# Performance work log

Measured on AMD Instinct MI355X. Metric: run time of the kernel, lower is better.

The kernel has to match this reference:

```python
import jax, jax.numpy as jnp
import numpy as np
import math

MODEL_DIM = 2048
NUM_EXPERTS = 64
N_TOKENS = 16384
CAPACITY_FACTOR = 1.0
MIN_CAPACITY = 8
THRESHOLD = 0.5


def _threshold_gating(logits):
    # Faithful jax translation of main_thresholdGating (training path, threshold>0).
    # Note: the torch code truncates sorted columns to the data-dependent
    # explore_top_k_num; we keep the full E columns instead. This is exactly
    # equivalent: dropped columns are all-unchosen (importance 0), and using
    # arange(E,0,-1) instead of arange(K,0,-1) shifts every chosen importance
    # by the same constant (E-K), which preserves the per-expert top-k order.
    N, E = logits.shape
    capacity = max(int(math.ceil(N / E * CAPACITY_FACTOR)), MIN_CAPACITY)  # static

    gates = jax.nn.softmax(logits, axis=1)                    # [N,E]
    indices1 = jnp.argmax(gates, axis=1)                      # top-1 expert per token
    mask1 = jax.nn.one_hot(indices1, E, dtype=gates.dtype)    # [N,E]

    # sorted gates + cumsum threshold selection
    gates_sorted, gates_idx = jax.lax.top_k(gates, E)         # [N,E] descending
    cum = jnp.cumsum(gates_sorted, axis=-1)
    chosen = (cum - gates_sorted) < THRESHOLD                 # [N,E] bool
    chosen = chosen.at[:, 0].set(True)                        # always keep top-1

    # scatter importance = rank-priority + gate prob into expert columns
    rank_imp = jnp.arange(E, 0, -1, dtype=gates.dtype)[None, :] + gates_sorted
    imp = jnp.where(chosen, rank_imp, jnp.zeros_like(rank_imp))
    row = jnp.arange(N)[:, None]
    # gates_idx rows are permutations of experts -> no scatter collisions
    tam = jnp.zeros((N, E), gates.dtype).at[row, gates_idx].set(imp)  # [N,E]

    # capacity truncation: per expert column keep the `capacity` tokens with
    # highest importance
    top_idx = jax.lax.top_k(tam.T, capacity)[1]               # [E, capacity]
    keep = jnp.zeros((N, E), gates.dtype).at[top_idx, jnp.arange(E)[:, None]].set(1.0)
    final_mask = ((tam * keep) > 0).astype(gates.dtype)       # [N,E]

    combine_weights = gates * final_mask

    # load-balancing aux loss (GShard style)
    me = jnp.mean(gates, axis=0)
    ce = jnp.mean(mask1, axis=0)
    l_aux = jnp.sum(me * ce) * E
    return l_aux, combine_weights


def setup_inputs() -> dict:
    key = jax.random.key(0)
    kx, kw = jax.random.split(key)
    x = jax.random.normal(kx, (N_TOKENS, MODEL_DIM), dtype=jnp.float32)
    # gate weight of wg = Linear(model_dim, num_experts, bias=False)
    W = jax.random.normal(kw, (NUM_EXPERTS, MODEL_DIM), dtype=jnp.float32) / math.sqrt(MODEL_DIM)
    return {"x": x, "W": W}


def reference(x, W):
    logits = x @ W.T                                          # [N,E]
    l_aux, combine_weights = _threshold_gating(logits)
    return l_aux, combine_weights
```

## Files before the change

kernel.cpp:

```cpp
#include <hip/hip_runtime.h>
#include <cstdint>
#include <cstddef>

#define N_TOK  16384
#define NEXP   64
#define KDIM   2048
#define CAP    256
#define NE_TOT ((size_t)N_TOK * NEXP)

typedef __attribute__((ext_vector_type(8))) short short8;
typedef __attribute__((ext_vector_type(4))) float f32x4;
typedef __attribute__((ext_vector_type(4))) unsigned int uint4x;

__device__ __forceinline__ unsigned short bf16_rtn(float f) {
  unsigned u = __float_as_uint(f);
  u += 0x7FFFu + ((u >> 16) & 1u);
  return (unsigned short)(u >> 16);
}
__device__ __forceinline__ float bf16_f(unsigned short h) {
  return __uint_as_float((unsigned)h << 16);
}
__device__ __forceinline__ f32x4 MF(short8 a, short8 b, f32x4 c) {
  return __builtin_amdgcn_mfma_f32_16x16x32_bf16(a, b, c, 0, 0, 0);
}
__device__ __forceinline__ unsigned cvt_pk(float a, float b) {
  unsigned r;
  asm("v_cvt_pk_bf16_f32 %0, %1, %2" : "=v"(r) : "v"(a), "v"(b));
  return r;
}
__device__ __forceinline__ float lo16f(unsigned u) {
  return __uint_as_float(u << 16);
}
__device__ __forceinline__ float hi16f(unsigned u) {
  return __uint_as_float(u & 0xFFFF0000u);
}

__global__ __launch_bounds__(256) void wdigits(const float* __restrict__ W,
    unsigned short* __restrict__ Wh, unsigned short* __restrict__ Wl,
    unsigned short* __restrict__ Wq) {
  const int e = (int)blockIdx.x * 256 + (int)threadIdx.x;
  const int col = e >> 11;
  const int k   = e & 2047;
  const float w = W[(size_t)col * KDIM + k];
  const unsigned short h = bf16_rtn(w);
  const float r1 = w - bf16_f(h);
  const unsigned short lo = bf16_rtn(r1);
  const float r2 = r1 - bf16_f(lo);
  const unsigned short q = bf16_rtn(r2);
  const size_t idx = (size_t)(k >> 3) * 512 + (size_t)col * 8 + (k & 7);
  Wh[idx] = h; Wl[idx] = lo; Wq[idx] = q;
}

__device__ __forceinline__ void cvt8pk(float4 a, float4 b,
                                       short8& h, short8& lo, short8& q) {
  const float f0 = a.x, f1 = a.y, f2 = a.z, f3 = a.w;
  const float f4 = b.x, f5 = b.y, f6 = b.z, f7 = b.w;
  const unsigned h0 = cvt_pk(f0, f1), h1 = cvt_pk(f2, f3);
  const unsigned h2 = cvt_pk(f4, f5), h3 = cvt_pk(f6, f7);
  const float r0 = f0 - lo16f(h0), r1 = f1 - hi16f(h0);
  const float r2 = f2 - lo16f(h1), r3 = f3 - hi16f(h1);
  const float r4 = f4 - lo16f(h2), r5 = f5 - hi16f(h2);
  const float r6 = f6 - lo16f(h3), r7 = f7 - hi16f(h3);
  const unsigned l0 = cvt_pk(r0, r1), l1 = cvt_pk(r2, r3);
  const unsigned l2 = cvt_pk(r4, r5), l3 = cvt_pk(r6, r7);
  const float s0 = r0 - lo16f(l0), s1 = r1 - hi16f(l0);
  const float s2 = r2 - lo16f(l1), s3 = r3 - hi16f(l1);
  const float s4 = r4 - lo16f(l2), s5 = r5 - hi16f(l2);
  const float s6 = r6 - lo16f(l3), s7 = r7 - hi16f(l3);
  const unsigned q0 = cvt_pk(s0, s1), q1 = cvt_pk(s2, s3);
  const unsigned q2 = cvt_pk(s4, s5), q3 = cvt_pk(s6, s7);
  h  = __builtin_bit_cast(short8, (uint4x){h0, h1, h2, h3});
  lo = __builtin_bit_cast(short8, (uint4x){l0, l1, l2, l3});
  q  = __builtin_bit_cast(short8, (uint4x){q0, q1, q2, q3});
}

template <int KS>
__global__ __launch_bounds__(256) void gemm_mfma(const float* __restrict__ x,
    const unsigned short* __restrict__ Wh, const unsigned short* __restrict__ Wl,
    const unsigned short* __restrict__ Wq, float* __restrict__ part) {
  constexpr int NSTEP = (KDIM / KS) / 32;
  const int tid = (int)threadIdx.x;
  const int l   = tid & 63;
  const int wv  = tid >> 6;
  const int ks  = (int)blockIdx.x % KS;
  const int mt  = (int)blockIdx.x / KS;
  const int row0 = mt * 256 + wv * 64;
  const int kBeg = ks * (KDIM / KS);
  const int lr = l & 15;
  const int lk = l >> 4;

  f32x4 acc[4][4];
#pragma unroll
  for (int rt = 0; rt < 4; ++rt)
#pragma unroll
    for (int cb = 0; cb < 4; ++cb) acc[rt][cb] = (f32x4){0.f, 0.f, 0.f, 0.f};

  const float* pa0 = x + (size_t)(row0 + lr) * KDIM + kBeg + lk * 8;
  const size_t bbase = ((size_t)((kBeg >> 3) + lk)) * 64 + lr;
  const short8* BH = (const short8*)Wh + bbase;
  const short8* BL = (const short8*)Wl + bbase;
  const short8* BQ = (const short8*)Wq + bbase;

  float4 Ac[4][2];
#pragma unroll
  for (int rt = 0; rt < 4; ++rt) {
    const float* p = pa0 + (size_t)rt * 16 * KDIM;
    Ac[rt][0] = *(const float4*)p;
    Ac[rt][1] = *(const float4*)(p + 4);
  }

  for (int s = 0; s < NSTEP; ++s) {
    const int so = s * 256;
    short8 bh[4], bl[4], bq[4];
#pragma unroll
    for (int cb = 0; cb < 4; ++cb) {
      bh[cb] = BH[so + cb * 16];
      bl[cb] = BL[so + cb * 16];
      bq[cb] = BQ[so + cb * 16];
    }
    float4 An[4][2];
    if (s + 1 < NSTEP) {
      const int ko = (s + 1) * 32;
#pragma unroll
      for (int rt = 0; rt < 4; ++rt) {
        const float* p = pa0 + (size_t)rt * 16 * KDIM + ko;
        An[rt][0] = *(const float4*)p;
        An[rt][1] = *(const float4*)(p + 4);
      }
    }
    short8 ah[4], al[4], aq[4];
#pragma unroll
    for (int rt = 0; rt < 4; ++rt)
      cvt8pk(Ac[rt][0], Ac[rt][1], ah[rt], al[rt], aq[rt]);

#pragma unroll
    for (int cb = 0; cb < 4; ++cb) {
#pragma unroll
      for (int rt = 0; rt < 4; ++rt) {
        acc[rt][cb] = MF(ah[rt], bh[cb], acc[rt][cb]);
        acc[rt][cb] = MF(ah[rt], bl[cb], acc[rt][cb]);
        acc[rt][cb] = MF(al[rt], bh[cb], acc[rt][cb]);
        acc[rt][cb] = MF(al[rt], bl[cb], acc[rt][cb]);
        acc[rt][cb] = MF(aq[rt], bh[cb], acc[rt][cb]);
        acc[rt][cb] = MF(ah[rt], bq[cb], acc[rt][cb]);
      }
    }

    if (s + 1 < NSTEP) {
#pragma unroll
      for (int rt = 0; rt < 4; ++rt) { Ac[rt][0] = An[rt][0]; Ac[rt][1] = An[rt][1]; }
    }
  }

  float* pout = part + (size_t)ks * NE_TOT;
#pragma unroll
  for (int rt = 0; rt < 4; ++rt) {
    const int rb = row0 + rt * 16 + lk * 4;
#pragma unroll
    for (int r = 0; r < 4; ++r) {
#pragma unroll
      for (int cb = 0; cb < 4; ++cb)
        pout[(size_t)(rb + r) * 64 + cb * 16 + lr] = acc[rt][cb][r];
    }
  }
}

template <int KS>
__global__ __launch_bounds__(1024) void gate_rows(const float* __restrict__ part,
                                                  float* __restrict__ gatesT,
                                                  float* __restrict__ tamT) {
  __shared__ float gt[64][65];
  __shared__ float tt[64][65];
  const int tid  = (int)threadIdx.x;
  const int lane = tid & 63;
  const int wid  = tid >> 6;
  const int row0 = (int)blockIdx.x * 64;

#pragma unroll
  for (int r = 0; r < 4; ++r) {
    const int rloc = wid * 4 + r;
    const size_t base = (size_t)(row0 + rloc) * NEXP;

    float logit = 0.f;
#pragma unroll
    for (int s = 0; s < KS; ++s)
      logit += part[(size_t)s * NE_TOT + base + lane];

    float m = logit;
#pragma unroll
    for (int off = 32; off > 0; off >>= 1) m = fmaxf(m, __shfl_xor(m, off));
    float p = expf(logit - m);
    float sum = p;
#pragma unroll
    for (int off = 32; off > 0; off >>= 1) sum += __shfl_xor(sum, off);
    const float gate = p / sum;

    float g = gate;
    int idx = lane;
#pragma unroll
    for (int k = 2; k <= 64; k <<= 1) {
#pragma unroll
      for (int j = k >> 1; j > 0; j >>= 1) {
        float og = __shfl_xor(g, j);
        int   oi = __shfl_xor(idx, j);
        bool iLower     = (lane & j) == 0;
        bool wantFirst  = ((lane & k) == 0) ? iLower : !iLower;
        bool otherFirst = (og > g) || (og == g && oi < idx);
        if (otherFirst == wantFirst) { g = og; idx = oi; }
      }
    }

    float cum = g;
#pragma unroll
    for (int off = 1; off < 64; off <<= 1) {
      float t = __shfl_up(cum, off);
      if (lane >= off) cum += t;
    }
    const bool chosen = (lane == 0) || ((cum - g) < 0.5f);
    const float imp = chosen ? ((float)(NEXP - lane) + g) : 0.f;

    gt[rloc][lane] = gate;
    tt[rloc][idx]  = imp;
  }
  __syncthreads();

#pragma unroll
  for (int p = 0; p < 4; ++p) {
    const int e = p * 16 + wid;
    gatesT[(size_t)e * N_TOK + row0 + lane] = gt[lane][e];
    tamT  [(size_t)e * N_TOK + row0 + lane] = tt[lane][e];
  }
}

__global__ __launch_bounds__(1024) void expert_select(
    const float* __restrict__ gatesT, const float* __restrict__ tamT,
    float* __restrict__ me_sum, int* __restrict__ ce_cnt,
    float* __restrict__ combT) {
  __shared__ int   hist16[16][256];
  __shared__ int   hist[256];
  __shared__ float wsum[16];
  __shared__ int   wice[16];
  __shared__ int   wnnz[16];
  __shared__ int   wcnt[16];
  __shared__ unsigned sh_prefix;
  __shared__ int      sh_k;
  __shared__ int      sh_nnz;

  const int e    = (int)blockIdx.x;
  const int tid  = (int)threadIdx.x;
  const int lane = tid & 63;
  const int wid  = tid >> 6;
  const float* tcol = tamT   + (size_t)e * N_TOK;
  const float* gcol = gatesT + (size_t)e * N_TOK;

  float gsum = 0.f;
  int ccnt = 0, nnzl = 0;
#pragma unroll
  for (int k = 0; k < 4; ++k) {
    int i4 = tid + k * 1024;
    float4 tv = reinterpret_cast<const float4*>(tcol)[i4];
    float4 gv = reinterpret_cast<const float4*>(gcol)[i4];
    gsum += gv.x + gv.y + gv.z + gv.w;
    ccnt += (tv.x > 64.f) + (tv.y > 64.f) + (tv.z > 64.f) + (tv.w > 64.f);
    nnzl += (tv.x != 0.f) + (tv.y != 0.f) + (tv.z != 0.f) + (tv.w != 0.f);
  }
#pragma unroll
  for (int off = 32; off > 0; off >>= 1) {
    gsum += __shfl_xor(gsum, off);
    ccnt += __shfl_xor(ccnt, off);
    nnzl += __shfl_xor(nnzl, off);
  }
  if (lane == 0) { wsum[wid] = gsum; wice[wid] = ccnt; wnnz[wid] = nnzl; }
  __syncthreads();
  if (tid == 0) {
    float t = 0.f; int c = 0, nz = 0;
    for (int w = 0; w < 16; ++w) { t += wsum[w]; c += wice[w]; nz += wnnz[w]; }
    me_sum[e] = t; ce_cnt[e] = c; sh_nnz = nz;
  }
  __syncthreads();
  const int nnz = sh_nnz;

  unsigned vstar = 0u;
  int meq = 0;
  if (nnz > CAP) {
    unsigned prefix = 0;
    int krem = CAP;
    for (int round = 0; round < 4; ++round) {
      const int shift = 24 - 8 * round;
      const unsigned maskAbove =
          (round == 0) ? 0u : (0xFFFFFFFFu << (shift + 8));
      for (int z = tid; z < 16 * 256; z += 1024) ((int*)hist16)[z] = 0;
      __syncthreads();
#pragma unroll
      for (int k = 0; k < 16; ++k) {
        unsigned u = __float_as_uint(tcol[tid + k * 1024]);
        if (u != 0u && (u & maskAbove) == prefix)
          atomicAdd(&hist16[wid][(u >> shift) & 255], 1);
      }
      __syncthreads();
      if (tid < 256) {
        int s = 0;
#pragma unroll
        for (int w = 0; w < 16; ++w) s += hist16[w][tid];
        hist[tid] = s;
      }
      __syncthreads();
      if (wid == 0) {
        int h0 = hist[lane * 4 + 0], h1 = hist[lane * 4 + 1];
        int h2 = hist[lane * 4 + 2], h3 = hist[lane * 4 + 3];
        int lsum = h0 + h1 + h2 + h3;
        int suf = lsum;
#pragma unroll
        for (int off = 1; off < 64; off <<= 1) {
          int t = __shfl_down(suf, off);
          if (lane + off < 64) suf += t;
        }
        int above = suf - lsum;
        int S3 = above + h3, S2 = S3 + h2, S1 = S2 + h1, S0 = S1 + h0;
        if (S0 >= krem && S1    < krem) { sh_prefix = prefix | ((unsigned)(lane*4+0) << shift); sh_k = krem - S1;    }
        if (S1 >= krem && S2    < krem) { sh_prefix = prefix | ((unsigned)(lane*4+1) << shift); sh_k = krem - S2;    }
        if (S2 >= krem && S3    < krem) { sh_prefix = prefix | ((unsigned)(lane*4+2) << shift); sh_k = krem - S3;    }
        if (S3 >= krem && above < krem) { sh_prefix = prefix | ((unsigned)(lane*4+3) << shift); sh_k = krem - above; }
      }
      __syncthreads();
      prefix = sh_prefix;
      krem   = sh_k;
      __syncthreads();
    }
    vstar = prefix;
    meq   = krem;
  }

  float4 tq[4];
#pragma unroll
  for (int q = 0; q < 4; ++q)
    tq[q] = reinterpret_cast<const float4*>(tcol)[tid * 4 + q];
  int cnt = 0;
#pragma unroll
  for (int q = 0; q < 4; ++q) {
    cnt += (__float_as_uint(tq[q].x) == vstar);
    cnt += (__float_as_uint(tq[q].y) == vstar);
    cnt += (__float_as_uint(tq[q].z) == vstar);
    cnt += (__float_as_uint(tq[q].w) == vstar);
  }
  int inc = cnt;
#pragma unroll
  for (int off = 1; off < 64; off <<= 1) {
    int t = __shfl_up(inc, off);
    if (lane >= off) inc += t;
  }
  if (lane == 63) wcnt[wid] = inc;
  __syncthreads();
  if (tid == 0) {
    int run = 0;
    for (int w = 0; w < 16; ++w) { int t = wcnt[w]; wcnt[w] = run; run += t; }
  }
  __syncthreads();
  int exc = (inc - cnt) + wcnt[wid];

  float* ccol = combT + (size_t)e * N_TOK;
#pragma unroll
  for (int q = 0; q < 4; ++q) {
    float4 gq = reinterpret_cast<const float4*>(gcol)[tid * 4 + q];
    float ov[4];
    const float tv[4] = {tq[q].x, tq[q].y, tq[q].z, tq[q].w};
    const float gv[4] = {gq.x, gq.y, gq.z, gq.w};
#pragma unroll
    for (int j = 0; j < 4; ++j) {
      unsigned u = __float_as_uint(tv[j]);
      bool keep;
      if (u == vstar) { keep = (exc < meq); ++exc; }
      else            { keep = (u > vstar); }
      ov[j] = (keep && u != 0u) ? gv[j] : 0.f;
    }
    reinterpret_cast<float4*>(ccol)[tid * 4 + q] =
        make_float4(ov[0], ov[1], ov[2], ov[3]);
  }
}

__global__ __launch_bounds__(1024) void transpose_out(
    const float* __restrict__ combT, float* __restrict__ out1,
    const float* __restrict__ me_sum, const int* __restrict__ ce_cnt,
    float* __restrict__ out0) {
  __shared__ float tile[64][65];
  const int tid  = (int)threadIdx.x;
  const int lane = tid & 63;
  const int wid  = tid >> 6;
  const int tok0 = (int)blockIdx.x * 64;
#pragma unroll
  for (int p = 0; p < 4; ++p) {
    const int e = p * 16 + wid;
    tile[lane][e] = combT[(size_t)e * N_TOK + tok0 + lane];
  }
  __syncthreads();
#pragma unroll
  for (int q = 0; q < 4; ++q) {
    const int tok = q * 16 + wid;
    out1[(size_t)(tok0 + tok) * NEXP + lane] = tile[tok][lane];
  }
  if (blockIdx.x == 0 && wid == 0) {
    float v = (me_sum[lane] / (float)N_TOK) *
              ((float)ce_cnt[lane] / (float)N_TOK);
#pragma unroll
    for (int off = 32; off > 0; off >>= 1) v += __shfl_xor(v, off);
    if (lane == 0) out0[0] = v * (float)NEXP;
  }
}

extern "C" void kernel_launch(void* const* d_in, const int* in_sizes, int n_in,
                              void* d_out, int out_size, void* d_ws, size_t ws_size,
                              hipStream_t stream) {
  const float* x = (const float*)d_in[0];
  const float* W = (const float*)d_in[1];
  float* out = (float*)d_out;
  float* ws  = (float*)d_ws;

  const bool ks8 = ws_size >= (size_t)(8 + 2) * NE_TOT * 4 + 1024;

  const int KS = ks8 ? 8 : 4;
  float* part   = ws;
  float* combT  = ws;
  float* gatesT = ws + (size_t)KS * NE_TOT;
  float* tamT   = gatesT + NE_TOT;
  float* me     = tamT + NE_TOT;
  int*   ce     = (int*)(me + 64);

  unsigned short* Wh = (unsigned short*)gatesT;
  unsigned short* Wl = Wh + (size_t)NEXP * KDIM;
  unsigned short* Wq = Wl + (size_t)NEXP * KDIM;

  wdigits<<<(NEXP * KDIM) / 256, 256, 0, stream>>>(W, Wh, Wl, Wq);
  if (ks8) gemm_mfma<8><<<64 * 8, 256, 0, stream>>>(x, Wh, Wl, Wq, part);
  else     gemm_mfma<4><<<64 * 4, 256, 0, stream>>>(x, Wh, Wl, Wq, part);
  if (ks8) gate_rows<8><<<N_TOK / 64, 1024, 0, stream>>>(part, gatesT, tamT);
  else     gate_rows<4><<<N_TOK / 64, 1024, 0, stream>>>(part, gatesT, tamT);
  expert_select<<<NEXP, 1024, 0, stream>>>(gatesT, tamT, me, ce, combT);
  transpose_out<<<N_TOK / 64, 1024, 0, stream>>>(combT, out + 1, me, ce, out);
}
```

Measured before the change: 73.95 us.

## Stage x tile through double-buffered LDS with coalesced global loads

```diff
diff --git a/kernel.cpp b/kernel.cpp
--- a/kernel.cpp
+++ b/kernel.cpp
@@ -79,13 +79,15 @@
     const unsigned short* __restrict__ Wh, const unsigned short* __restrict__ Wl,
     const unsigned short* __restrict__ Wq, float* __restrict__ part) {
   constexpr int NSTEP = (KDIM / KS) / 32;
+  __shared__ float As[2][9216];
   const int tid = (int)threadIdx.x;
   const int l   = tid & 63;
   const int wv  = tid >> 6;
   const int ks  = (int)blockIdx.x % KS;
   const int mt  = (int)blockIdx.x / KS;
-  const int row0 = mt * 256 + wv * 64;
-  const int kBeg = ks * (KDIM / KS);
+  const int row0b = mt * 256;
+  const int row0  = row0b + wv * 64;
+  const int kBeg  = ks * (KDIM / KS);
   const int lr = l & 15;
   const int lk = l >> 4;
 
@@ -95,21 +97,32 @@
 #pragma unroll
     for (int cb = 0; cb < 4; ++cb) acc[rt][cb] = (f32x4){0.f, 0.f, 0.f, 0.f};
 
-  const float* pa0 = x + (size_t)(row0 + lr) * KDIM + kBeg + lk * 8;
+  const int sgr = tid >> 3;
+  const int sch = tid & 7;
+  const float* sp = x + (size_t)(row0b + sgr) * KDIM + kBeg + sch * 4;
+
   const size_t bbase = ((size_t)((kBeg >> 3) + lk)) * 64 + lr;
   const short8* BH = (const short8*)Wh + bbase;
   const short8* BL = (const short8*)Wl + bbase;
   const short8* BQ = (const short8*)Wq + bbase;
 
-  float4 Ac[4][2];
-#pragma unroll
-  for (int rt = 0; rt < 4; ++rt) {
-    const float* p = pa0 + (size_t)rt * 16 * KDIM;
-    Ac[rt][0] = *(const float4*)p;
-    Ac[rt][1] = *(const float4*)(p + 4);
-  }
+  float4 st[8];
+#pragma unroll
+  for (int p = 0; p < 8; ++p)
+    st[p] = *(const float4*)(sp + (size_t)p * 32 * KDIM);
+#pragma unroll
+  for (int p = 0; p < 8; ++p)
+    *(float4*)&As[0][(sgr + p * 32) * 36 + sch * 4] = st[p];
+  __syncthreads();
 
   for (int s = 0; s < NSTEP; ++s) {
+    const int buf = s & 1;
+    if (s + 1 < NSTEP) {
+      const int ko = (s + 1) * 32;
+#pragma unroll
+      for (int p = 0; p < 8; ++p)
+        st[p] = *(const float4*)(sp + (size_t)p * 32 * KDIM + ko);
+    }
     const int so = s * 256;
     short8 bh[4], bl[4], bq[4];
 #pragma unroll
@@ -118,20 +131,14 @@
       bl[cb] = BL[so + cb * 16];
       bq[cb] = BQ[so + cb * 16];
     }
-    float4 An[4][2];
-    if (s + 1 < NSTEP) {
-      const int ko = (s + 1) * 32;
-#pragma unroll
-      for (int rt = 0; rt < 4; ++rt) {
-        const float* p = pa0 + (size_t)rt * 16 * KDIM + ko;
-        An[rt][0] = *(const float4*)p;
-        An[rt][1] = *(const float4*)(p + 4);
-      }
-    }
     short8 ah[4], al[4], aq[4];
 #pragma unroll
-    for (int rt = 0; rt < 4; ++rt)
-      cvt8pk(Ac[rt][0], Ac[rt][1], ah[rt], al[rt], aq[rt]);
+    for (int rt = 0; rt < 4; ++rt) {
+      const float* pb = &As[buf][(wv * 64 + rt * 16 + lr) * 36 + lk * 8];
+      float4 A0 = *(const float4*)pb;
+      float4 A1 = *(const float4*)(pb + 4);
+      cvt8pk(A0, A1, ah[rt], al[rt], aq[rt]);
+    }
 
 #pragma unroll
     for (int cb = 0; cb < 4; ++cb) {
@@ -148,8 +155,10 @@
 
     if (s + 1 < NSTEP) {
 #pragma unroll
-      for (int rt = 0; rt < 4; ++rt) { Ac[rt][0] = An[rt][0]; Ac[rt][1] = An[rt][1]; }
-    }
+      for (int p = 0; p < 8; ++p)
+        *(float4*)&As[buf ^ 1][(sgr + p * 32) * 36 + sch * 4] = st[p];
+    }
+    __syncthreads();
   }
 
   float* pout = part + (size_t)ks * NE_TOT;
```

Measured after the change: 87.41 us. 1.18x slower.

## Stage x tiles through LDS with async global_load_lds double buffering

Applied to the files above, without the earlier changes.

```diff
diff --git a/kernel.cpp b/kernel.cpp
--- a/kernel.cpp
+++ b/kernel.cpp
@@ -79,6 +79,7 @@
     const unsigned short* __restrict__ Wh, const unsigned short* __restrict__ Wl,
     const unsigned short* __restrict__ Wq, float* __restrict__ part) {
   constexpr int NSTEP = (KDIM / KS) / 32;
+  __shared__ float xs[2][4][2048];
   const int tid = (int)threadIdx.x;
   const int l   = tid & 63;
   const int wv  = tid >> 6;
@@ -95,21 +96,36 @@
 #pragma unroll
     for (int cb = 0; cb < 4; ++cb) acc[rt][cb] = (f32x4){0.f, 0.f, 0.f, 0.f};
 
-  const float* pa0 = x + (size_t)(row0 + lr) * KDIM + kBeg + lk * 8;
+  const int srow = l >> 3;
+  const int sch  = (l & 7) ^ srow;
+  const float* sp = x + (size_t)(row0 + srow) * KDIM + kBeg + sch * 4;
+
+  const int m7  = lr & 7;
+  const int c0o = ((lk * 2)     ^ m7) * 4;
+  const int c1o = ((lk * 2 + 1) ^ m7) * 4;
+
   const size_t bbase = ((size_t)((kBeg >> 3) + lk)) * 64 + lr;
   const short8* BH = (const short8*)Wh + bbase;
   const short8* BL = (const short8*)Wl + bbase;
   const short8* BQ = (const short8*)Wq + bbase;
 
-  float4 Ac[4][2];
-#pragma unroll
-  for (int rt = 0; rt < 4; ++rt) {
-    const float* p = pa0 + (size_t)rt * 16 * KDIM;
-    Ac[rt][0] = *(const float4*)p;
-    Ac[rt][1] = *(const float4*)(p + 4);
-  }
+#define STAGE(buf, koff)                                                     \
+  {                                                                          \
+    _Pragma("unroll")                                                        \
+    for (int i_ = 0; i_ < 8; ++i_) {                                         \
+      __builtin_amdgcn_global_load_lds(                                      \
+          sp + (size_t)(i_ * 8) * KDIM + (koff),                             \
+          &xs[(buf)][wv][i_ * 256], 16, 0, 0);                               \
+    }                                                                        \
+  }
+
+  STAGE(0, 0)
+  __syncthreads();
 
   for (int s = 0; s < NSTEP; ++s) {
+    const int buf = s & 1;
+    if (s + 1 < NSTEP) STAGE(buf ^ 1, (s + 1) * 32)
+
     const int so = s * 256;
     short8 bh[4], bl[4], bq[4];
 #pragma unroll
@@ -118,20 +134,15 @@
       bl[cb] = BL[so + cb * 16];
       bq[cb] = BQ[so + cb * 16];
     }
-    float4 An[4][2];
-    if (s + 1 < NSTEP) {
-      const int ko = (s + 1) * 32;
-#pragma unroll
-      for (int rt = 0; rt < 4; ++rt) {
-        const float* p = pa0 + (size_t)rt * 16 * KDIM + ko;
-        An[rt][0] = *(const float4*)p;
-        An[rt][1] = *(const float4*)(p + 4);
-      }
-    }
+
     short8 ah[4], al[4], aq[4];
 #pragma unroll
-    for (int rt = 0; rt < 4; ++rt)
-      cvt8pk(Ac[rt][0], Ac[rt][1], ah[rt], al[rt], aq[rt]);
+    for (int rt = 0; rt < 4; ++rt) {
+      const float* pb = &xs[buf][wv][(rt * 16 + lr) * 32];
+      float4 A0 = *(const float4*)(pb + c0o);
+      float4 A1 = *(const float4*)(pb + c1o);
+      cvt8pk(A0, A1, ah[rt], al[rt], aq[rt]);
+    }
 
 #pragma unroll
     for (int cb = 0; cb < 4; ++cb) {
@@ -146,11 +157,9 @@
       }
     }
 
-    if (s + 1 < NSTEP) {
-#pragma unroll
-      for (int rt = 0; rt < 4; ++rt) { Ac[rt][0] = An[rt][0]; Ac[rt][1] = An[rt][1]; }
-    }
-  }
+    __syncthreads();
+  }
+#undef STAGE
 
   float* pout = part + (size_t)ks * NE_TOT;
 #pragma unroll
```

New measurement: 74.36 us. About the same (+0.6%).
